# Kernel optimization log

Measured on AMD Instinct MI355X. Metric: run time of the kernel, lower is better.

Reference implementation:

```python
import jax, jax.numpy as jnp
import numpy as np

K = 16384   # num_particles
IN = 512    # input_size
H = 1024    # hidden_size
ALPHA = 0.5 # resamp_alpha


def setup_inputs() -> dict:
    key = jax.random.key(0)
    ks = jax.random.split(key, 16)
    s = 0.02
    return {
        'input_': jax.random.normal(ks[0], (1, IN), jnp.float32),
        'h0': jax.random.uniform(ks[1], (K, H), jnp.float32),
        'p0': jax.random.normal(ks[2], (K, 1), jnp.float32),
        'eps': jax.random.normal(ks[3], (K, H), jnp.float32),
        'w_z': jax.random.normal(ks[4], (H + IN, H), jnp.float32) * s,
        'b_z': jnp.zeros((H,), jnp.float32),
        'w_r': jax.random.normal(ks[5], (H + IN, H), jnp.float32) * s,
        'b_r': jnp.zeros((H,), jnp.float32),
        'w_n': jax.random.normal(ks[6], (H + IN, 2 * H), jnp.float32) * s,
        'b_n': jnp.zeros((2 * H,), jnp.float32),
        'w_obs': jax.random.normal(ks[7], (H + IN, 1), jnp.float32) * s,
        'b_obs': jnp.zeros((1,), jnp.float32),
        'w_h1': jax.random.normal(ks[8], (H, 24), jnp.float32) * s,
        'b_h1': jnp.zeros((24,), jnp.float32),
        'w_h2': jax.random.normal(ks[9], (24, 2), jnp.float32) * s,
        'b_h2': jnp.zeros((2,), jnp.float32),
    }


def reference(input_, h0, p0, eps, w_z, b_z, w_r, b_r, w_n, b_n,
              w_obs, b_obs, w_h1, b_h1, w_h2, b_h2):
    # obs_in = input_.repeat(num_particles, 1)
    obs_in = jnp.broadcast_to(input_, (K, IN))          # [K, IN]
    obs_cat = jnp.concatenate([h0, obs_in], axis=1)     # [K, H+IN]
    z = jax.nn.sigmoid(obs_cat @ w_z + b_z)             # [K, H]
    r = jax.nn.sigmoid(obs_cat @ w_r + b_r)             # [K, H]
    n_pre = jnp.concatenate([r * h0, obs_in], axis=1) @ w_n + b_n  # [K, 2H]
    mu_n, var_n = n_pre[:, :H], n_pre[:, H:]
    # reparameterize: std = softplus(var), sample = mu + eps * std
    n = jnp.tanh(mu_n + eps * jax.nn.softplus(var_n))   # activation == 'tanh'
    h1 = (1.0 - z) * n + z * h0                         # [K, H]
    # observation likelihood -> normalized log weights over particles
    logpdf = jnp.concatenate([h1, obs_in], axis=1) @ w_obs + b_obs  # [K, 1]
    p1 = jax.nn.log_softmax(logpdf + p0, axis=0)        # [K, 1]
    # soft resampling (torch.multinomial with replacement)
    resamp_prob = ALPHA * jnp.exp(p1[:, 0]) + (1.0 - ALPHA) / K     # [K]
    idx = jax.random.categorical(jax.random.key(42), jnp.log(resamp_prob), shape=(K,))
    h1 = h1[idx]                                         # [K, H] gather
    pn = jnp.exp(p1[idx, 0])
    pn = pn / (ALPHA * pn + (1.0 - ALPHA) / K)
    pn = jnp.log(pn)
    p1 = (pn - jax.nn.logsumexp(pn, axis=0))[:, None]    # [K, 1]
    # exp-weighted reduce + small MLP head (dropout p=0 is identity)
    mean_hid = jnp.sum(jnp.exp(p1) * h1, axis=0)         # [H]
    loc_pred = jnp.maximum(mean_hid @ w_h1 + b_h1, 0.0) @ w_h2 + b_h2  # [2]
    return loc_pred, h1, p1
```

## Files before the change

### kernel.cpp

```cpp
#include <hip/hip_runtime.h>
#include <math.h>
#include <stdint.h>

#define KP 16384
#define IN_DIM 512
#define HD 1024
#define WQ 512
#define HOTCAP 1024

typedef _Float16 f16x8 __attribute__((ext_vector_type(8)));
typedef float f32x4 __attribute__((ext_vector_type(4)));

__device__ __forceinline__ uint32_t rotl(uint32_t x, uint32_t r) {
  return __builtin_amdgcn_alignbit(x, x, 32u - r);
}

__device__ __forceinline__ uint32_t tf_bits(uint32_t x1) {
  const uint32_t ks1 = 42u, ks2 = 42u ^ 0x1BD11BDAu;
  uint32_t x0 = x1;
  x1 = rotl(x1, 13) ^ x0;
  x0 += x1; x1 = rotl(x1, 15) ^ x0;
  x0 += x1; x1 = rotl(x1, 26) ^ x0;
  x0 += x1; x1 = rotl(x1, 6)  ^ x0;
  x0 += ks1; x1 += ks2 + 1u;
  x0 += x1; x1 = rotl(x1, 17) ^ x0;
  x0 += x1; x1 = rotl(x1, 29) ^ x0;
  x0 += x1; x1 = rotl(x1, 16) ^ x0;
  x0 += x1; x1 = rotl(x1, 24) ^ x0;
  x0 += ks2; x1 += 2u;
  x0 += x1; x1 = rotl(x1, 13) ^ x0;
  x0 += x1; x1 = rotl(x1, 15) ^ x0;
  x0 += x1; x1 = rotl(x1, 26) ^ x0;
  x0 += x1; x1 = rotl(x1, 6)  ^ x0;
  x1 += ks1 + 3u;
  x0 += x1; x1 = rotl(x1, 17) ^ x0;
  x0 += x1; x1 = rotl(x1, 29) ^ x0;
  x0 += x1; x1 = rotl(x1, 16) ^ x0;
  x0 += x1; x1 = rotl(x1, 24) ^ x0;
  x0 += ks1; x1 += ks2 + 4u;
  x0 += x1; x1 = rotl(x1, 13) ^ x0;
  x0 += x1; x1 = rotl(x1, 15) ^ x0;
  x0 += x1; x1 = rotl(x1, 26) ^ x0;
  x0 += x1; x1 = rotl(x1, 6)  ^ x0;
  x0 += ks2; x1 += 5u;
  return x0 ^ x1;
}

__device__ __forceinline__ float gumbel_from_bits(uint32_t b) {
  uint32_t ub = (b >> 9) | 0x3f800000u;
  float u = __uint_as_float(ub) - 1.0f;
  u = fmaxf(u, 1.1754943508222875e-38f);
  return -logf(-logf(u));
}

__device__ __forceinline__ unsigned long long pack_key(float g, int c) {
  uint32_t u = __float_as_uint(g);
  u = (u & 0x80000000u) ? ~u : (u | 0x80000000u);
  return ((unsigned long long)u << 32) | (uint32_t)(16383 - c);
}

__global__ __launch_bounds__(256) void bias_kernel(
    const float* __restrict__ in,
    const float* __restrict__ wz, const float* __restrict__ bz,
    const float* __restrict__ wr, const float* __restrict__ br,
    const float* __restrict__ wn, const float* __restrict__ bn,
    const float* __restrict__ wobs, const float* __restrict__ bobs,
    float* __restrict__ zb, float* __restrict__ rb,
    float* __restrict__ nb, float* __restrict__ ob) {
  __shared__ float sin_[IN_DIM];
  int t = threadIdx.x;
  for (int i = t; i < IN_DIM; i += 256) sin_[i] = in[i];
  __syncthreads();
  int gid = blockIdx.x * 256 + t;
  if (gid < 1024) {
    float s = bz[gid];
    for (int i = 0; i < IN_DIM; ++i) s = fmaf(sin_[i], wz[(HD + i) * HD + gid], s);
    zb[gid] = s;
  } else if (gid < 2048) {
    int j = gid - 1024;
    float s = br[j];
    for (int i = 0; i < IN_DIM; ++i) s = fmaf(sin_[i], wr[(HD + i) * HD + j], s);
    rb[j] = s;
  } else if (gid < 4096) {
    int j = gid - 2048;
    float s = bn[j];
    for (int i = 0; i < IN_DIM; ++i) s = fmaf(sin_[i], wn[(HD + i) * 2048 + j], s);
    nb[j] = s;
  } else if (gid == 4096) {
    float s = bobs[0];
    for (int i = 0; i < IN_DIM; ++i) s = fmaf(sin_[i], wobs[HD + i], s);
    ob[0] = s;
  }
}

__global__ __launch_bounds__(256) void splitw_kernel(
    const float* __restrict__ wz, const float* __restrict__ wr,
    const float* __restrict__ wn,
    _Float16* __restrict__ zHi, _Float16* __restrict__ zLo,
    _Float16* __restrict__ rHi, _Float16* __restrict__ rLo,
    _Float16* __restrict__ mHi, _Float16* __restrict__ mLo,
    _Float16* __restrict__ vHi, _Float16* __restrict__ vLo) {
  __shared__ float tile[32][33];
  int m = blockIdx.z;
  const float* src; int ld, cofs; _Float16 *oh, *ol;
  if (m == 0)      { src = wz; ld = 1024; cofs = 0;    oh = zHi; ol = zLo; }
  else if (m == 1) { src = wr; ld = 1024; cofs = 0;    oh = rHi; ol = rLo; }
  else if (m == 2) { src = wn; ld = 2048; cofs = 0;    oh = mHi; ol = mLo; }
  else             { src = wn; ld = 2048; cofs = 1024; oh = vHi; ol = vLo; }
  int k0 = blockIdx.x * 32, n0 = blockIdx.y * 32;
  int tx = threadIdx.x & 31, ty = threadIdx.x >> 5;
#pragma unroll
  for (int i = 0; i < 4; ++i) {
    int k = ty * 4 + i;
    tile[k][tx] = src[(size_t)(k0 + k) * ld + cofs + n0 + tx];
  }
  __syncthreads();
#pragma unroll
  for (int i = 0; i < 4; ++i) {
    int n = ty * 4 + i;
    float v = tile[tx][n] * 64.0f;
    _Float16 h = (_Float16)v;
    _Float16 l = (_Float16)((v - (float)h) * 2048.0f);
    oh[(size_t)(n0 + n) * 1024 + k0 + tx] = h;
    ol[(size_t)(n0 + n) * 1024 + k0 + tx] = l;
  }
}

#define LDH 40

__global__ __launch_bounds__(256, 2) void gemm_zr_mfma(
    const float* __restrict__ A,
    const _Float16* __restrict__ BzHi, const _Float16* __restrict__ BzLo,
    const _Float16* __restrict__ BrHi, const _Float16* __restrict__ BrLo,
    const float* __restrict__ zbias, const float* __restrict__ rbias,
    float* __restrict__ zout,
    _Float16* __restrict__ rhh, _Float16* __restrict__ rhl) {
  __shared__ __align__(16) _Float16 Ah[128 * LDH], Al[128 * LDH];
  __shared__ __align__(16) _Float16 B0h[64 * LDH], B0l[64 * LDH];
  __shared__ __align__(16) _Float16 B1h[64 * LDH], B1l[64 * LDH];
  int t = threadIdx.x;
  int row0 = blockIdx.x * 128, col0 = blockIdx.y * 64;
  int wave = t >> 6, lane = t & 63;
  int lr = lane & 15, hh = lane >> 4;
  int WR = (wave >> 1) * 64, WC = (wave & 1) * 32;

  f32x4 acc0[4][2][2] = {};
  f32x4 acc1[4][2][2] = {};

  for (int kb = 0; kb < 1024; kb += 32) {
#pragma unroll
    for (int p = 0; p < 2; ++p) {
      int id = t + p * 256;
      int row = id >> 2, kc = id & 3;
      const float* g = &A[(size_t)(row0 + row) * 1024 + kb + kc * 8];
      float4 v0 = *(const float4*)g;
      float4 v1 = *(const float4*)(g + 4);
      float vv[8] = {v0.x, v0.y, v0.z, v0.w, v1.x, v1.y, v1.z, v1.w};
      f16x8 hi, lo;
#pragma unroll
      for (int j = 0; j < 8; ++j) {
        _Float16 h = (_Float16)vv[j];
        hi[j] = h;
        lo[j] = (_Float16)((vv[j] - (float)h) * 2048.0f);
      }
      *(f16x8*)&Ah[row * LDH + kc * 8] = hi;
      *(f16x8*)&Al[row * LDH + kc * 8] = lo;
    }
    {
      int n = t >> 2, kc = t & 3;
      size_t gofs = (size_t)(col0 + n) * 1024 + kb + kc * 8;
      int lofs = n * LDH + kc * 8;
      *(f16x8*)&B0h[lofs] = *(const f16x8*)&BzHi[gofs];
      *(f16x8*)&B0l[lofs] = *(const f16x8*)&BzLo[gofs];
      *(f16x8*)&B1h[lofs] = *(const f16x8*)&BrHi[gofs];
      *(f16x8*)&B1l[lofs] = *(const f16x8*)&BrLo[gofs];
    }
    __syncthreads();
    f16x8 ah[4], al[4], bh[2][2], bl[2][2];
#pragma unroll
    for (int mt = 0; mt < 4; ++mt) {
      int r = WR + mt * 16 + lr;
      ah[mt] = *(f16x8*)&Ah[r * LDH + hh * 8];
      al[mt] = *(f16x8*)&Al[r * LDH + hh * 8];
    }
#pragma unroll
    for (int nt = 0; nt < 2; ++nt) {
      int c = WC + nt * 16 + lr;
      bh[0][nt] = *(f16x8*)&B0h[c * LDH + hh * 8];
      bl[0][nt] = *(f16x8*)&B0l[c * LDH + hh * 8];
      bh[1][nt] = *(f16x8*)&B1h[c * LDH + hh * 8];
      bl[1][nt] = *(f16x8*)&B1l[c * LDH + hh * 8];
    }
#pragma unroll
    for (int mt = 0; mt < 4; ++mt)
#pragma unroll
      for (int nt = 0; nt < 2; ++nt)
#pragma unroll
        for (int m = 0; m < 2; ++m) {
          acc0[mt][nt][m] = __builtin_amdgcn_mfma_f32_16x16x32_f16(ah[mt], bh[m][nt], acc0[mt][nt][m], 0, 0, 0);
          acc1[mt][nt][m] = __builtin_amdgcn_mfma_f32_16x16x32_f16(ah[mt], bl[m][nt], acc1[mt][nt][m], 0, 0, 0);
          acc1[mt][nt][m] = __builtin_amdgcn_mfma_f32_16x16x32_f16(al[mt], bh[m][nt], acc1[mt][nt][m], 0, 0, 0);
        }
    __syncthreads();
  }
  const float INV = 1.0f / 2048.0f, WS = 1.0f / 64.0f;
#pragma unroll
  for (int mt = 0; mt < 4; ++mt)
#pragma unroll
    for (int nt = 0; nt < 2; ++nt) {
      int col = col0 + WC + nt * 16 + lr;
#pragma unroll
      for (int q = 0; q < 4; ++q) {
        int row = row0 + WR + mt * 16 + hh * 4 + q;
        size_t off = (size_t)row * 1024 + col;
        float vz = (acc0[mt][nt][0][q] + acc1[mt][nt][0][q] * INV) * WS + zbias[col];
        float vr = (acc0[mt][nt][1][q] + acc1[mt][nt][1][q] * INV) * WS + rbias[col];
        float z = 1.0f / (1.0f + expf(-vz));
        float r = 1.0f / (1.0f + expf(-vr));
        float rv = r * A[off];
        zout[off] = z;
        _Float16 rhi = (_Float16)rv;
        rhh[off] = rhi;
        rhl[off] = (_Float16)((rv - (float)rhi) * 2048.0f);
      }
    }
}

__global__ __launch_bounds__(256, 2) void gemm_n_mfma(
    const _Float16* __restrict__ Ahg, const _Float16* __restrict__ Alg,
    const _Float16* __restrict__ BmHi, const _Float16* __restrict__ BmLo,
    const _Float16* __restrict__ BvHi, const _Float16* __restrict__ BvLo,
    const float* __restrict__ nbias,
    const float* __restrict__ h0, const float* __restrict__ eps,
    const float* __restrict__ zbuf, float* __restrict__ h1out) {
  __shared__ __align__(16) _Float16 Ah[128 * LDH], Al[128 * LDH];
  __shared__ __align__(16) _Float16 B0h[64 * LDH], B0l[64 * LDH];
  __shared__ __align__(16) _Float16 B1h[64 * LDH], B1l[64 * LDH];
  int t = threadIdx.x;
  int row0 = blockIdx.x * 128, col0 = blockIdx.y * 64;
  int wave = t >> 6, lane = t & 63;
  int lr = lane & 15, hh = lane >> 4;
  int WR = (wave >> 1) * 64, WC = (wave & 1) * 32;

  f32x4 acc0[4][2][2] = {};
  f32x4 acc1[4][2][2] = {};

  for (int kb = 0; kb < 1024; kb += 32) {
#pragma unroll
    for (int p = 0; p < 2; ++p) {
      int id = t + p * 256;
      int row = id >> 2, kc = id & 3;
      size_t g = (size_t)(row0 + row) * 1024 + kb + kc * 8;
      int lofs = row * LDH + kc * 8;
      *(f16x8*)&Ah[lofs] = *(const f16x8*)&Ahg[g];
      *(f16x8*)&Al[lofs] = *(const f16x8*)&Alg[g];
    }
    {
      int n = t >> 2, kc = t & 3;
      size_t gofs = (size_t)(col0 + n) * 1024 + kb + kc * 8;
      int lofs = n * LDH + kc * 8;
      *(f16x8*)&B0h[lofs] = *(const f16x8*)&BmHi[gofs];
      *(f16x8*)&B0l[lofs] = *(const f16x8*)&BmLo[gofs];
      *(f16x8*)&B1h[lofs] = *(const f16x8*)&BvHi[gofs];
      *(f16x8*)&B1l[lofs] = *(const f16x8*)&BvLo[gofs];
    }
    __syncthreads();
    f16x8 ah[4], al[4], bh[2][2], bl[2][2];
#pragma unroll
    for (int mt = 0; mt < 4; ++mt) {
      int r = WR + mt * 16 + lr;
      ah[mt] = *(f16x8*)&Ah[r * LDH + hh * 8];
      al[mt] = *(f16x8*)&Al[r * LDH + hh * 8];
    }
#pragma unroll
    for (int nt = 0; nt < 2; ++nt) {
      int c = WC + nt * 16 + lr;
      bh[0][nt] = *(f16x8*)&B0h[c * LDH + hh * 8];
      bl[0][nt] = *(f16x8*)&B0l[c * LDH + hh * 8];
      bh[1][nt] = *(f16x8*)&B1h[c * LDH + hh * 8];
      bl[1][nt] = *(f16x8*)&B1l[c * LDH + hh * 8];
    }
#pragma unroll
    for (int mt = 0; mt < 4; ++mt)
#pragma unroll
      for (int nt = 0; nt < 2; ++nt)
#pragma unroll
        for (int m = 0; m < 2; ++m) {
          acc0[mt][nt][m] = __builtin_amdgcn_mfma_f32_16x16x32_f16(ah[mt], bh[m][nt], acc0[mt][nt][m], 0, 0, 0);
          acc1[mt][nt][m] = __builtin_amdgcn_mfma_f32_16x16x32_f16(ah[mt], bl[m][nt], acc1[mt][nt][m], 0, 0, 0);
          acc1[mt][nt][m] = __builtin_amdgcn_mfma_f32_16x16x32_f16(al[mt], bh[m][nt], acc1[mt][nt][m], 0, 0, 0);
        }
    __syncthreads();
  }
  const float INV = 1.0f / 2048.0f, WS = 1.0f / 64.0f;
#pragma unroll
  for (int mt = 0; mt < 4; ++mt)
#pragma unroll
    for (int nt = 0; nt < 2; ++nt) {
      int col = col0 + WC + nt * 16 + lr;
#pragma unroll
      for (int q = 0; q < 4; ++q) {
        int row = row0 + WR + mt * 16 + hh * 4 + q;
        size_t off = (size_t)row * 1024 + col;
        float mu = (acc0[mt][nt][0][q] + acc1[mt][nt][0][q] * INV) * WS + nbias[col];
        float var = (acc0[mt][nt][1][q] + acc1[mt][nt][1][q] * INV) * WS + nbias[1024 + col];
        float sp = fmaxf(var, 0.0f) + log1pf(expf(-fabsf(var)));
        float n = tanhf(mu + eps[off] * sp);
        float z = zbuf[off];
        h1out[off] = (1.0f - z) * n + z * h0[off];
      }
    }
}

__global__ __launch_bounds__(256) void score_kernel(
    const float* __restrict__ h1, const float* __restrict__ wobs,
    const float* __restrict__ ob, const float* __restrict__ p0,
    float* __restrict__ s) {
  __shared__ float w[HD];
  int t = threadIdx.x;
  for (int i = t; i < HD; i += 256) w[i] = wobs[i];
  __syncthreads();
  int wave = t >> 6, lane = t & 63;
  int row = blockIdx.x * 4 + wave;
  float acc = 0.0f;
  for (int c = lane * 4; c < HD; c += 256) {
    float4 v = *(const float4*)&h1[(size_t)row * HD + c];
    acc = fmaf(v.x, w[c], acc);
    acc = fmaf(v.y, w[c + 1], acc);
    acc = fmaf(v.z, w[c + 2], acc);
    acc = fmaf(v.w, w[c + 3], acc);
  }
#pragma unroll
  for (int off = 32; off; off >>= 1) acc += __shfl_down(acc, off);
  if (lane == 0) s[row] = acc + ob[0] + p0[row];
}

__global__ __launch_bounds__(1024) void softmax_kernel(
    const float* __restrict__ s, float* __restrict__ p1v,
    float* __restrict__ logits, float* __restrict__ lmaxp,
    int* __restrict__ hotc, unsigned int* __restrict__ hotn) {
  __shared__ float red[1024];
  int t = threadIdx.x;
  if (t == 0) hotn[0] = 0u;
  float m = -INFINITY;
  for (int k = t; k < KP; k += 1024) m = fmaxf(m, s[k]);
  red[t] = m; __syncthreads();
  for (int o = 512; o; o >>= 1) { if (t < o) red[t] = fmaxf(red[t], red[t + o]); __syncthreads(); }
  m = red[0]; __syncthreads();
  float sum = 0.0f;
  for (int k = t; k < KP; k += 1024) sum += expf(s[k] - m);
  red[t] = sum; __syncthreads();
  for (int o = 512; o; o >>= 1) { if (t < o) red[t] += red[t + o]; __syncthreads(); }
  float ls = logf(red[0]);
  float lmax = logf(0.5f * expf(-ls) + (0.5f / KP));
  float hthr = lmax - 6.0f;
  for (int k = t; k < KP; k += 1024) {
    float p = s[k] - m - ls;
    p1v[k] = p;
    float lg = logf(0.5f * expf(p) + (0.5f / KP));
    logits[k] = lg;
    if (lg > hthr) {
      unsigned int slot = atomicAdd(hotn, 1u);
      if (slot < HOTCAP) hotc[slot] = k;
    }
  }
  if (t == 0) lmaxp[0] = lmax;
}

__global__ __launch_bounds__(256) void thr_kernel(
    const float* __restrict__ logits, const float* __restrict__ lmaxp,
    const int* __restrict__ hotc, const unsigned int* __restrict__ hotn,
    uint32_t* __restrict__ sthr, unsigned long long* __restrict__ best) {
  int t = threadIdx.x;
  int wave = t >> 6, lane = t & 63;
  int r = blockIdx.x * 4 + wave;
  uint32_t base = ((uint32_t)r << 14) + 42u;

  unsigned long long key = 0ull;
#pragma unroll
  for (int j = 0; j < 4; ++j) {
    int c = lane + j * 64;
    uint32_t bits = tf_bits(base + (uint32_t)c);
    float g = gumbel_from_bits(bits) + logits[c];
    unsigned long long k2 = pack_key(g, c);
    if (k2 > key) key = k2;
  }
  int hn = (int)hotn[0];
  if (hn > HOTCAP) hn = HOTCAP;
  for (int i = lane; i < hn; i += 64) {
    int c = hotc[i];
    uint32_t bits = tf_bits(base + (uint32_t)c);
    float g = gumbel_from_bits(bits) + logits[c];
    unsigned long long k2 = pack_key(g, c);
    if (k2 > key) key = k2;
  }
#pragma unroll
  for (int off = 32; off; off >>= 1) {
    unsigned long long ok = __shfl_down(key, off);
    if (ok > key) key = ok;
  }
  if (lane == 0) {
    uint32_t u = (uint32_t)(key >> 32);
    u = (u & 0x80000000u) ? (u & 0x7FFFFFFFu) : ~u;
    float B0 = __uint_as_float(u);
    float wth = expf(lmaxp[0] + 1e-3f - B0);
    float omu = -expm1f(-wth);
    float delta = 8388608.0f * omu;
    uint32_t thr;
    if (delta >= 8388592.0f) thr = 0u;
    else {
      thr = 8388608u - (uint32_t)delta;
      thr = (thr > 24u) ? (thr - 24u) : 0u;
    }
    sthr[r] = thr << 9;
    best[r] = key;
  }
}

__global__ __launch_bounds__(256) void scan_kernel(
    const uint32_t* __restrict__ sthr, const float* __restrict__ logits,
    const unsigned long long* __restrict__ best, int* __restrict__ idx) {
  __shared__ uint32_t qb[4][WQ];
  __shared__ uint32_t qc[4][WQ];
  __shared__ unsigned long long redw[4];
  int t = threadIdx.x;
  int wave = t >> 6, lane = t & 63;
  int r = blockIdx.x;
  uint32_t thr = sthr[r];
  uint32_t base = ((uint32_t)r << 14) + 42u;

  unsigned long long mykey = 0ull;
  int wcnt = 0;
  for (int it = 0; it < 63; ++it) {
    uint32_t c = 256u + (uint32_t)it * 256u + (uint32_t)t;
    uint32_t bits = tf_bits(base + c);
    bool pass = bits >= thr;
    unsigned long long mball = __ballot(pass);
    if (mball) {
      int pos = __popcll(mball & ((1ull << lane) - 1ull));
      if (pass) {
        int slot = wcnt + pos;
        if (slot < WQ) { qb[wave][slot] = bits; qc[wave][slot] = c; }
        else {
          float g = gumbel_from_bits(bits) + logits[c];
          unsigned long long kk = pack_key(g, (int)c);
          if (kk > mykey) mykey = kk;
        }
      }
      wcnt += __popcll(mball);
    }
  }
  int n = wcnt < WQ ? wcnt : WQ;
  for (int i = lane; i < n; i += 64) {
    float g = gumbel_from_bits(qb[wave][i]) + logits[qc[wave][i]];
    unsigned long long kk = pack_key(g, (int)qc[wave][i]);
    if (kk > mykey) mykey = kk;
  }
#pragma unroll
  for (int off = 32; off; off >>= 1) {
    unsigned long long ok = __shfl_down(mykey, off);
    if (ok > mykey) mykey = ok;
  }
  if (lane == 0) redw[wave] = mykey;
  __syncthreads();
  if (t == 0) {
    unsigned long long k = best[r];
    for (int w = 0; w < 4; ++w) if (redw[w] > k) k = redw[w];
    idx[r] = 16383 - (int)(k & 16383ull);
  }
}

__global__ __launch_bounds__(1024) void resample_kernel(
    const float* __restrict__ p1v, const int* __restrict__ idx,
    float* __restrict__ pn, float* __restrict__ p1out, float* __restrict__ wexp) {
  __shared__ float red[1024];
  int t = threadIdx.x;
  float m = -INFINITY;
  for (int k = t; k < KP; k += 1024) {
    float pv = p1v[idx[k]];
    float w = expf(pv);
    float v = logf(w / (0.5f * w + (0.5f / KP)));
    pn[k] = v;
    m = fmaxf(m, v);
  }
  red[t] = m; __syncthreads();
  for (int o = 512; o; o >>= 1) { if (t < o) red[t] = fmaxf(red[t], red[t + o]); __syncthreads(); }
  m = red[0]; __syncthreads();
  float sum = 0.0f;
  for (int k = t; k < KP; k += 1024) sum += expf(pn[k] - m);
  red[t] = sum; __syncthreads();
  for (int o = 512; o; o >>= 1) { if (t < o) red[t] += red[t + o]; __syncthreads(); }
  float lse = m + logf(red[0]);
  for (int k = t; k < KP; k += 1024) {
    float v = pn[k] - lse;
    p1out[k] = v;
    wexp[k] = expf(v);
  }
}

__global__ __launch_bounds__(256) void gather_kernel(
    const float* __restrict__ h1pre, const int* __restrict__ idx,
    const float* __restrict__ wexp, float* __restrict__ h1out,
    float* __restrict__ partials) {
  int t = threadIdx.x;
  int k0 = blockIdx.x * 64;
  float part[4] = {0.f, 0.f, 0.f, 0.f};
  for (int kk = 0; kk < 64; ++kk) {
    int k = k0 + kk;
    int src = idx[k];
    float w = wexp[k];
#pragma unroll
    for (int c = 0; c < 4; ++c) {
      float v = h1pre[(size_t)src * HD + t + c * 256];
      h1out[(size_t)k * HD + t + c * 256] = v;
      part[c] = fmaf(w, v, part[c]);
    }
  }
#pragma unroll
  for (int c = 0; c < 4; ++c) partials[(size_t)blockIdx.x * HD + t + c * 256] = part[c];
}

__global__ __launch_bounds__(256) void reduce_mean_kernel(
    const float* __restrict__ partials, float* __restrict__ mean_hid) {
  int j = blockIdx.x * 256 + threadIdx.x;
  float s = 0.0f;
  for (int b = 0; b < 256; ++b) s += partials[(size_t)b * HD + j];
  mean_hid[j] = s;
}

__global__ __launch_bounds__(64) void final_kernel(
    const float* __restrict__ mean_hid,
    const float* __restrict__ wh1, const float* __restrict__ bh1,
    const float* __restrict__ wh2, const float* __restrict__ bh2,
    float* __restrict__ out) {
  __shared__ float hrelu[24];
  int t = threadIdx.x;
  if (t < 24) {
    float s = bh1[t];
    for (int i = 0; i < HD; ++i) s = fmaf(mean_hid[i], wh1[i * 24 + t], s);
    hrelu[t] = fmaxf(s, 0.0f);
  }
  __syncthreads();
  if (t < 2) {
    float s = bh2[t];
    for (int j = 0; j < 24; ++j) s = fmaf(hrelu[j], wh2[j * 2 + t], s);
    out[t] = s;
  }
}

extern "C" void kernel_launch(void* const* d_in, const int* in_sizes, int n_in,
                              void* d_out, int out_size, void* d_ws, size_t ws_size,
                              hipStream_t stream) {
  (void)in_sizes; (void)n_in; (void)out_size; (void)ws_size;
  const float* input_ = (const float*)d_in[0];
  const float* h0    = (const float*)d_in[1];
  const float* p0    = (const float*)d_in[2];
  const float* eps   = (const float*)d_in[3];
  const float* w_z   = (const float*)d_in[4];
  const float* b_z   = (const float*)d_in[5];
  const float* w_r   = (const float*)d_in[6];
  const float* b_r   = (const float*)d_in[7];
  const float* w_n   = (const float*)d_in[8];
  const float* b_n   = (const float*)d_in[9];
  const float* w_obs = (const float*)d_in[10];
  const float* b_obs = (const float*)d_in[11];
  const float* w_h1  = (const float*)d_in[12];
  const float* b_h1  = (const float*)d_in[13];
  const float* w_h2  = (const float*)d_in[14];
  const float* b_h2  = (const float*)d_in[15];

  float* out = (float*)d_out;
  float* out_loc = out;
  float* out_h1  = out + 2;
  float* out_p1  = out + 2 + (size_t)KP * HD;

  _Float16* rhh  = (_Float16*)d_ws;
  _Float16* rhl  = rhh + (size_t)KP * HD;
  float* h1pre   = (float*)(rhl + (size_t)KP * HD);
  float* zb      = h1pre + (size_t)KP * HD;
  float* rb      = zb + 1024;
  float* nb      = rb + 1024;
  float* ob      = nb + 2048;
  float* sbuf    = ob + 16;
  float* p1v     = sbuf + KP;
  float* logits  = p1v + KP;
  float* pn      = logits + KP;
  float* wexpb   = pn + KP;
  float* mean_hid= wexpb + KP;
  float* partials= mean_hid + 1024;
  int*   idxb    = (int*)(partials + 256 * HD);
  uint32_t* sthrb = (uint32_t*)(idxb + KP);
  unsigned long long* bestb = (unsigned long long*)(sthrb + KP);
  int*   hotcb   = (int*)(bestb + KP);
  unsigned int* hotnb = (unsigned int*)(hotcb + HOTCAP);
  _Float16* wt   = (_Float16*)(hotnb + 16);
  _Float16* wzHi = wt;
  _Float16* wzLo = wt + 1 * (size_t)HD * HD;
  _Float16* wrHi = wt + 2 * (size_t)HD * HD;
  _Float16* wrLo = wt + 3 * (size_t)HD * HD;
  _Float16* wmHi = wt + 4 * (size_t)HD * HD;
  _Float16* wmLo = wt + 5 * (size_t)HD * HD;
  _Float16* wvHi = wt + 6 * (size_t)HD * HD;
  _Float16* wvLo = wt + 7 * (size_t)HD * HD;

  bias_kernel<<<17, 256, 0, stream>>>(input_, w_z, b_z, w_r, b_r, w_n, b_n,
                                      w_obs, b_obs, zb, rb, nb, ob);

  dim3 gs(32, 32, 4);
  splitw_kernel<<<gs, 256, 0, stream>>>(w_z, w_r, w_n, wzHi, wzLo, wrHi, wrLo,
                                        wmHi, wmLo, wvHi, wvLo);

  dim3 g1(KP / 128, HD / 64);
  gemm_zr_mfma<<<g1, 256, 0, stream>>>(h0, wzHi, wzLo, wrHi, wrLo, zb, rb,
                                       out_h1 , rhh, rhl);

  gemm_n_mfma<<<g1, 256, 0, stream>>>(rhh, rhl, wmHi, wmLo, wvHi, wvLo, nb,
                                      h0, eps, out_h1 , h1pre);

  score_kernel<<<KP / 4, 256, 0, stream>>>(h1pre, w_obs, ob, p0, sbuf);

  softmax_kernel<<<1, 1024, 0, stream>>>(sbuf, p1v, logits, ob + 8, hotcb, hotnb);

  thr_kernel<<<KP / 4, 256, 0, stream>>>(logits, ob + 8, hotcb, hotnb, sthrb, bestb);

  scan_kernel<<<KP, 256, 0, stream>>>(sthrb, logits, bestb, idxb);

  resample_kernel<<<1, 1024, 0, stream>>>(p1v, idxb, pn, out_p1, wexpb);

  gather_kernel<<<KP / 64, 256, 0, stream>>>(h1pre, idxb, wexpb, out_h1, partials);

  reduce_mean_kernel<<<4, 256, 0, stream>>>(partials, mean_hid);

  final_kernel<<<1, 64, 0, stream>>>(mean_hid, w_h1, b_h1, w_h2, b_h2, out_loc);
}
```

Measured before the change: 1.431 ms.

## Batch four rows per scan block and compact hot list with adaptive threshold

The Gumbel scan kernel now handles four resampling rows per block, 4096 blocks in place of 16384. Each thread hashes four consecutive columns per step to expose more independent threefry work, and the scan range now starts at column 0 instead of 256, which re-hashes the first 256 columns. The softmax kernel replaces the atomic hot-candidate append with a prefix-sum compaction. It also picks the largest margin below the max logit (2 to 10) whose candidate count fits in the hot buffer, so the hot list is deterministic and never overflows. This costs extra block-wide reductions and barriers in the single-block softmax and adds per-row barriers in the scan.

```diff
diff --git a/kernel.cpp b/kernel.cpp
--- a/kernel.cpp
+++ b/kernel.cpp
@@ -340,8 +340,9 @@
     float* __restrict__ logits, float* __restrict__ lmaxp,
     int* __restrict__ hotc, unsigned int* __restrict__ hotn) {
   __shared__ float red[1024];
-  int t = threadIdx.x;
-  if (t == 0) hotn[0] = 0u;
+  __shared__ int sc[1024];
+  __shared__ float sh_thr;
+  int t = threadIdx.x;
   float m = -INFINITY;
   for (int k = t; k < KP; k += 1024) m = fmaxf(m, s[k]);
   red[t] = m; __syncthreads();
@@ -353,17 +354,47 @@
   for (int o = 512; o; o >>= 1) { if (t < o) red[t] += red[t + o]; __syncthreads(); }
   float ls = logf(red[0]);
   float lmax = logf(0.5f * expf(-ls) + (0.5f / KP));
-  float hthr = lmax - 6.0f;
-  for (int k = t; k < KP; k += 1024) {
+
+  float lg[16];
+#pragma unroll
+  for (int j = 0; j < 16; ++j) {
+    int k = t * 16 + j;
     float p = s[k] - m - ls;
     p1v[k] = p;
-    float lg = logf(0.5f * expf(p) + (0.5f / KP));
-    logits[k] = lg;
-    if (lg > hthr) {
-      unsigned int slot = atomicAdd(hotn, 1u);
-      if (slot < HOTCAP) hotc[slot] = k;
-    }
-  }
+    lg[j] = logf(0.5f * expf(p) + (0.5f / KP));
+    logits[k] = lg[j];
+  }
+  float chosen = INFINITY;
+#pragma unroll
+  for (int d = 2; d <= 10; d += 2) {
+    float cand = lmax - (float)d;
+    int cnt = 0;
+#pragma unroll
+    for (int j = 0; j < 16; ++j) cnt += (lg[j] > cand) ? 1 : 0;
+    sc[t] = cnt; __syncthreads();
+    for (int o = 512; o; o >>= 1) { if (t < o) sc[t] += sc[t + o]; __syncthreads(); }
+    int total = sc[0]; __syncthreads();
+    if (total <= HOTCAP) chosen = cand;
+  }
+  if (t == 0) sh_thr = chosen;
+  __syncthreads();
+  float hthr = sh_thr;
+  int mycnt = 0;
+#pragma unroll
+  for (int j = 0; j < 16; ++j) mycnt += (lg[j] > hthr) ? 1 : 0;
+  sc[t] = mycnt; __syncthreads();
+  for (int o = 1; o < 1024; o <<= 1) {
+    int v = (t >= o) ? sc[t - o] : 0;
+    __syncthreads();
+    sc[t] += v;
+    __syncthreads();
+  }
+  int ofs = sc[t] - mycnt;
+#pragma unroll
+  for (int j = 0; j < 16; ++j) {
+    if (lg[j] > hthr) hotc[ofs++] = t * 16 + j;
+  }
+  if (t == 1023) hotn[0] = (unsigned int)sc[1023];
   if (t == 0) lmaxp[0] = lmax;
 }
 
@@ -425,48 +456,59 @@
   __shared__ unsigned long long redw[4];
   int t = threadIdx.x;
   int wave = t >> 6, lane = t & 63;
-  int r = blockIdx.x;
-  uint32_t thr = sthr[r];
-  uint32_t base = ((uint32_t)r << 14) + 42u;
-
-  unsigned long long mykey = 0ull;
-  int wcnt = 0;
-  for (int it = 0; it < 63; ++it) {
-    uint32_t c = 256u + (uint32_t)it * 256u + (uint32_t)t;
-    uint32_t bits = tf_bits(base + c);
-    bool pass = bits >= thr;
-    unsigned long long mball = __ballot(pass);
-    if (mball) {
-      int pos = __popcll(mball & ((1ull << lane) - 1ull));
-      if (pass) {
-        int slot = wcnt + pos;
-        if (slot < WQ) { qb[wave][slot] = bits; qc[wave][slot] = c; }
-        else {
-          float g = gumbel_from_bits(bits) + logits[c];
-          unsigned long long kk = pack_key(g, (int)c);
-          if (kk > mykey) mykey = kk;
-        }
-      }
-      wcnt += __popcll(mball);
-    }
-  }
-  int n = wcnt < WQ ? wcnt : WQ;
-  for (int i = lane; i < n; i += 64) {
-    float g = gumbel_from_bits(qb[wave][i]) + logits[qc[wave][i]];
-    unsigned long long kk = pack_key(g, (int)qc[wave][i]);
-    if (kk > mykey) mykey = kk;
-  }
-#pragma unroll
-  for (int off = 32; off; off >>= 1) {
-    unsigned long long ok = __shfl_down(mykey, off);
-    if (ok > mykey) mykey = ok;
-  }
-  if (lane == 0) redw[wave] = mykey;
-  __syncthreads();
-  if (t == 0) {
-    unsigned long long k = best[r];
-    for (int w = 0; w < 4; ++w) if (redw[w] > k) k = redw[w];
-    idx[r] = 16383 - (int)(k & 16383ull);
+  unsigned long long lmask = (1ull << lane) - 1ull;
+
+  for (int j = 0; j < 4; ++j) {
+    int r = blockIdx.x * 4 + j;
+    uint32_t thr = sthr[r];
+    uint32_t base = ((uint32_t)r << 14) + 42u;
+    unsigned long long mykey = 0ull;
+    int wcnt = 0;
+#pragma unroll 2
+    for (int k = 0; k < 16; ++k) {
+      uint32_t c0 = (uint32_t)k * 1024u + (uint32_t)t * 4u;
+      uint32_t v0 = base + c0;
+      uint32_t b0 = tf_bits(v0);
+      uint32_t b1 = tf_bits(v0 + 1u);
+      uint32_t b2 = tf_bits(v0 + 2u);
+      uint32_t b3 = tf_bits(v0 + 3u);
+#define QPUSH(bits, cc) {                                                 \
+      bool pass = (bits) >= thr;                                          \
+      unsigned long long mb = __ballot(pass);                             \
+      if (mb) {                                                           \
+        if (pass) {                                                       \
+          int slot = wcnt + __popcll(mb & lmask);                         \
+          if (slot < WQ) { qb[wave][slot] = (bits); qc[wave][slot] = (cc); } \
+          else { float g = gumbel_from_bits(bits) + logits[cc];           \
+                 unsigned long long kk = pack_key(g, (int)(cc));          \
+                 if (kk > mykey) mykey = kk; }                            \
+        }                                                                 \
+        wcnt += __popcll(mb); } }
+      QPUSH(b0, c0)
+      QPUSH(b1, c0 + 1u)
+      QPUSH(b2, c0 + 2u)
+      QPUSH(b3, c0 + 3u)
+#undef QPUSH
+    }
+    int n = wcnt < WQ ? wcnt : WQ;
+    for (int i = lane; i < n; i += 64) {
+      float g = gumbel_from_bits(qb[wave][i]) + logits[qc[wave][i]];
+      unsigned long long kk = pack_key(g, (int)qc[wave][i]);
+      if (kk > mykey) mykey = kk;
+    }
+#pragma unroll
+    for (int off = 32; off; off >>= 1) {
+      unsigned long long ok = __shfl_down(mykey, off);
+      if (ok > mykey) mykey = ok;
+    }
+    if (lane == 0) redw[wave] = mykey;
+    __syncthreads();
+    if (t == 0) {
+      unsigned long long k2 = best[r];
+      for (int w = 0; w < 4; ++w) if (redw[w] > k2) k2 = redw[w];
+      idx[r] = 16383 - (int)(k2 & 16383ull);
+    }
+    __syncthreads();
   }
 }
 
@@ -623,7 +665,7 @@
 
   thr_kernel<<<KP / 4, 256, 0, stream>>>(logits, ob + 8, hotcb, hotnb, sthrb, bestb);
 
-  scan_kernel<<<KP, 256, 0, stream>>>(sthrb, logits, bestb, idxb);
+  scan_kernel<<<4096, 256, 0, stream>>>(sthrb, logits, bestb, idxb);
 
   resample_kernel<<<1, 1024, 0, stream>>>(p1v, idxb, pn, out_p1, wexpb);
 
```

New measurement: 1.249 ms. 1.15x faster.
